# Performance work log

Measured on AMD Instinct MI355X. Metric: run time of the kernel, lower is better.

The kernel has to match this reference:

```python
import jax, jax.numpy as jnp
import numpy as np

N, IN_C, HID, OUT_C, DEPTH = 4096, 128, 256, 128, 3
KS = [2048, 1024, 512]  # ceil(0.5 * N_level)
E = 131072


def glorot(key, fan_in, fan_out):
    lim = np.sqrt(6.0 / (fan_in + fan_out))
    return jax.random.uniform(key, (fan_in, fan_out), jnp.float32, -lim, lim)


def build_adj(edge_index, n):
    # symmetric, self-loop-free adjacency with unit edge weights
    A = jnp.zeros((n, n), jnp.float32)
    A = A.at[edge_index[0], edge_index[1]].set(1.0)
    A = jnp.maximum(A, A.T)
    return A * (1.0 - jnp.eye(n, dtype=jnp.float32))


def gcn(x, A, W, b):
    # GCNConv(improved=True): A_hat = A + 2I, symmetric normalization
    n = A.shape[0]
    Ah = A + 2.0 * jnp.eye(n, dtype=A.dtype)
    deg = Ah.sum(axis=1)
    dinv = jnp.where(deg > 0, deg ** -0.5, 0.0)
    An = dinv[:, None] * Ah * dinv[None, :]
    return An @ (x @ W) + b


def augment(A):
    # remove self loops, add self loops (w=1), square (spspmm), remove self loops
    n = A.shape[0]
    I = jnp.eye(n, dtype=A.dtype)
    Al = A * (1.0 - I) + I
    A2 = Al @ Al
    return A2 * (1.0 - I)


def topk_pool(x, A, p, k):
    score = jnp.tanh((x @ p) / jnp.linalg.norm(p))
    vals, perm = jax.lax.top_k(score, k)
    return x[perm] * vals[:, None], A[perm][:, perm], perm


def setup_inputs() -> dict:
    key = jax.random.key(0)
    ks = jax.random.split(key, 16)
    x = jax.random.normal(ks[0], (N, IN_C), jnp.float32)
    edge_index = jax.random.randint(ks[1], (2, E), 0, N, jnp.int32)
    d = {"x": x, "edge_index": edge_index}
    d["Wd0"], d["bd0"] = glorot(ks[2], IN_C, HID), jnp.zeros((HID,), jnp.float32)
    d["Wd1"], d["bd1"] = glorot(ks[3], HID, HID), jnp.zeros((HID,), jnp.float32)
    d["Wd2"], d["bd2"] = glorot(ks[4], HID, HID), jnp.zeros((HID,), jnp.float32)
    d["Wd3"], d["bd3"] = glorot(ks[5], HID, HID), jnp.zeros((HID,), jnp.float32)
    d["p1"] = jax.random.normal(ks[6], (HID,), jnp.float32)
    d["p2"] = jax.random.normal(ks[7], (HID,), jnp.float32)
    d["p3"] = jax.random.normal(ks[8], (HID,), jnp.float32)
    d["Wu0"], d["bu0"] = glorot(ks[9], HID, HID), jnp.zeros((HID,), jnp.float32)
    d["Wu1"], d["bu1"] = glorot(ks[10], HID, HID), jnp.zeros((HID,), jnp.float32)
    d["Wu2"], d["bu2"] = glorot(ks[11], HID, OUT_C), jnp.zeros((OUT_C,), jnp.float32)
    return d


def reference(x, edge_index, Wd0, bd0, Wd1, bd1, Wd2, bd2, Wd3, bd3,
              p1, p2, p3, Wu0, bu0, Wu1, bu1, Wu2, bu2):
    n = x.shape[0]
    A = build_adj(edge_index, n)
    x = jax.nn.relu(gcn(x, A, Wd0, bd0))
    xs, As, perms = [x], [A], []
    down = [(Wd1, bd1), (Wd2, bd2), (Wd3, bd3)]
    pools = [p1, p2, p3]
    for i in range(DEPTH):
        A = augment(A)
        x, A, perm = topk_pool(x, A, pools[i], KS[i])
        x = jax.nn.relu(gcn(x, A, *down[i]))
        if i < DEPTH - 1:
            xs.append(x)
            As.append(A)
        perms.append(perm)
    up = [(Wu0, bu0), (Wu1, bu1), (Wu2, bu2)]
    for i in range(DEPTH):
        j = DEPTH - 1 - i
        res, perm = xs[j], perms[j]
        u = jnp.zeros_like(res).at[perm].set(x)
        x = res + u  # sum_res=True
        x = gcn(x, As[j], *up[i])
        if i < DEPTH - 1:
            x = jax.nn.relu(x)
    return x
```

## Files before the change

kernel.cpp:

```cpp
#include <hip/hip_runtime.h>


typedef __attribute__((ext_vector_type(8))) short bf16x8;
typedef __attribute__((ext_vector_type(4))) short s16x4;
typedef __attribute__((ext_vector_type(4))) float f32x4;

__device__ __forceinline__ short f2bf(float f) {
    unsigned u = __builtin_bit_cast(unsigned, f);
    u += 0x7FFFu + ((u >> 16) & 1u);
    return (short)(u >> 16);
}
__device__ __forceinline__ float bf2f(short s) {
    unsigned u = ((unsigned)(unsigned short)s) << 16;
    return __builtin_bit_cast(float, u);
}

#define GLL16(gsrc, ldst)                                                        \
    __builtin_amdgcn_global_load_lds(                                            \
        (__attribute__((address_space(1))) void*)(gsrc),                         \
        (__attribute__((address_space(3))) void*)(ldst), 16, 0, 0)

template<int MODE, int EPI>
__global__ __launch_bounds__(256, 2)
void gemm_bt(const short* __restrict__ Ah, const short* __restrict__ Al,
             const short* __restrict__ Bh, const short* __restrict__ Bl,
             float* __restrict__ Cf, int M, int N, int K, int kChunk)
{
    if (EPI == 1 && (int)blockIdx.y > (int)blockIdx.x) return;

    __shared__ short sAh[128 * 32];
    __shared__ short sBh[128 * 32];
    __shared__ short sAl[(MODE == 2) ? 128 * 32 : 8];
    __shared__ short sBl[(MODE >= 1) ? 128 * 32 : 8];

    const int t    = threadIdx.x;
    const int lane = t & 63;
    const int wave = t >> 6;
    const int tM   = blockIdx.y * 128;
    const int tN   = blockIdx.x * 128;
    const int k0   = blockIdx.z * kChunk;

    const int wm  = (wave >> 1) * 64;
    const int wn  = (wave & 1) * 64;
    const int l15 = lane & 15;
    const int g8  = (lane >> 4) * 8;

    f32x4 acc[4][4];
    const f32x4 zero = {0.f, 0.f, 0.f, 0.f};
#pragma unroll
    for (int i = 0; i < 4; i++)
#pragma unroll
        for (int j = 0; j < 4; j++) acc[i][j] = zero;

    const int i0 = t, i1 = t + 256;
    const short* a0 = Ah + (size_t)(tM + (i0 >> 2)) * K + (i0 & 3) * 8;
    const short* a1 = Ah + (size_t)(tM + (i1 >> 2)) * K + (i1 & 3) * 8;
    const short* b0 = Bh + (size_t)(tN + (i0 >> 2)) * K + (i0 & 3) * 8;
    const short* b1 = Bh + (size_t)(tN + (i1 >> 2)) * K + (i1 & 3) * 8;
    const short *bl0 = nullptr, *bl1 = nullptr, *al0 = nullptr, *al1 = nullptr;
    if (MODE >= 1) {
        bl0 = Bl + (size_t)(tN + (i0 >> 2)) * K + (i0 & 3) * 8;
        bl1 = Bl + (size_t)(tN + (i1 >> 2)) * K + (i1 & 3) * 8;
    }
    if (MODE == 2) {
        al0 = Al + (size_t)(tM + (i0 >> 2)) * K + (i0 & 3) * 8;
        al1 = Al + (size_t)(tM + (i1 >> 2)) * K + (i1 & 3) * 8;
    }

    for (int kb = k0; kb < k0 + kChunk; kb += 32) {
        GLL16(a0 + kb, &sAh[i0 * 8]);
        GLL16(a1 + kb, &sAh[i1 * 8]);
        GLL16(b0 + kb, &sBh[i0 * 8]);
        GLL16(b1 + kb, &sBh[i1 * 8]);
        if (MODE >= 1) { GLL16(bl0 + kb, &sBl[i0 * 8]); GLL16(bl1 + kb, &sBl[i1 * 8]); }
        if (MODE == 2) { GLL16(al0 + kb, &sAl[i0 * 8]); GLL16(al1 + kb, &sAl[i1 * 8]); }
        __syncthreads();

        bf16x8 aF[4], bF[4], aL[4], bL[4];
#pragma unroll
        for (int i = 0; i < 4; i++)
            aF[i] = *(const bf16x8*)&sAh[(wm + i * 16 + l15) * 32 + g8];
#pragma unroll
        for (int j = 0; j < 4; j++)
            bF[j] = *(const bf16x8*)&sBh[(wn + j * 16 + l15) * 32 + g8];
        if (MODE >= 1)
#pragma unroll
            for (int j = 0; j < 4; j++)
                bL[j] = *(const bf16x8*)&sBl[(wn + j * 16 + l15) * 32 + g8];
        if (MODE == 2)
#pragma unroll
            for (int i = 0; i < 4; i++)
                aL[i] = *(const bf16x8*)&sAl[(wm + i * 16 + l15) * 32 + g8];

#pragma unroll
        for (int i = 0; i < 4; i++)
#pragma unroll
            for (int j = 0; j < 4; j++) {
                acc[i][j] = __builtin_amdgcn_mfma_f32_16x16x32_bf16(aF[i], bF[j], acc[i][j], 0, 0, 0);
                if (MODE >= 1)
                    acc[i][j] = __builtin_amdgcn_mfma_f32_16x16x32_bf16(aF[i], bL[j], acc[i][j], 0, 0, 0);
                if (MODE == 2)
                    acc[i][j] = __builtin_amdgcn_mfma_f32_16x16x32_bf16(aL[i], bF[j], acc[i][j], 0, 0, 0);
            }
        __syncthreads();
    }

    const int r4 = (lane >> 4) * 4;
    if (EPI == 3) {
        float* CT = Cf + (size_t)blockIdx.z * M * N;
#pragma unroll
        for (int i = 0; i < 4; i++)
#pragma unroll
            for (int j = 0; j < 4; j++) {
                const int col   = tN + wn + j * 16 + l15;
                const int rbase = tM + wm + i * 16 + r4;
                *(f32x4*)&CT[(size_t)col * M + rbase] = acc[i][j];
            }
    } else {
        float* Cg = Cf + (size_t)blockIdx.z * M * N;
#pragma unroll
        for (int i = 0; i < 4; i++)
#pragma unroll
            for (int j = 0; j < 4; j++) {
                const int col = tN + wn + j * 16 + l15;
                float* cp = Cg + (size_t)(tM + wm + i * 16 + r4) * N + col;
#pragma unroll
                for (int r = 0; r < 4; r++) cp[(size_t)r * N] = acc[i][j][r];
            }
        if (EPI == 1 && tM != tN) {
#pragma unroll
            for (int i = 0; i < 4; i++)
#pragma unroll
                for (int j = 0; j < 4; j++) {
                    const int col   = tN + wn + j * 16 + l15;
                    const int rbase = tM + wm + i * 16 + r4;
                    *(f32x4*)&Cg[(size_t)col * N + rbase] = acc[i][j];
                }
        }
    }
}


__global__ void prep(const float* __restrict__ Wd0, const float* __restrict__ Wd1,
                     const float* __restrict__ Wd2, const float* __restrict__ Wd3,
                     const float* __restrict__ Wu0, const float* __restrict__ Wu1,
                     const float* __restrict__ Wu2, const float* __restrict__ x0,
                     short* __restrict__ Wth, short* __restrict__ Wtl,
                     short* __restrict__ Xh, short* __restrict__ Xl,
                     unsigned long long* __restrict__ M0)
{
    int t = blockIdx.x * 256 + threadIdx.x;
    float v; int dst;
    if (t < 32768)       { int e = t;          v = Wd0[e]; dst = 0      + (e & 255) * 128 + (e >> 8); }
    else if (t < 98304)  { int e = t - 32768;  v = Wd1[e]; dst = 32768  + (e & 255) * 256 + (e >> 8); }
    else if (t < 163840) { int e = t - 98304;  v = Wd2[e]; dst = 98304  + (e & 255) * 256 + (e >> 8); }
    else if (t < 229376) { int e = t - 163840; v = Wd3[e]; dst = 163840 + (e & 255) * 256 + (e >> 8); }
    else if (t < 294912) { int e = t - 229376; v = Wu0[e]; dst = 229376 + (e & 255) * 256 + (e >> 8); }
    else if (t < 360448) { int e = t - 294912; v = Wu1[e]; dst = 294912 + (e & 255) * 256 + (e >> 8); }
    else if (t < 393216) { int e = t - 360448; v = Wu2[e]; dst = 360448 + (e & 127) * 256 + (e >> 7); }
    else if (t < 917504) {
        int e = t - 393216;
        v = x0[e];
        short h = f2bf(v);
        Xh[e] = h; Xl[e] = f2bf(v - bf2f(h));
        return;
    } else {
        M0[t - 917504] = 0ull;
        return;
    }
    short h = f2bf(v);
    Wth[dst] = h; Wtl[dst] = f2bf(v - bf2f(h));
}

__global__ void build_bits(const int* __restrict__ ei, int E,
                           unsigned long long* __restrict__ M0)
{
    int e = blockIdx.x * 256 + threadIdx.x;
    if (e >= E) return;
    int i = ei[e], j = ei[E + e];
    if (i != j) {
        atomicOr(&M0[(size_t)i * 64 + (j >> 6)], 1ull << (j & 63));
        atomicOr(&M0[(size_t)j * 64 + (i >> 6)], 1ull << (i & 63));
    }
}

__global__ void row_compact_bits(const unsigned long long* __restrict__ M0,
                                 int* __restrict__ csr, float* __restrict__ rs)
{
    int row = blockIdx.x * 4 + (threadIdx.x >> 6);
    int lane = threadIdx.x & 63;
    unsigned long long w = M0[(size_t)row * 64 + lane];
    int c = __popcll(w);
    int incl = c;
    for (int off = 1; off < 64; off <<= 1) {
        int v = __shfl_up(incl, off);
        if (lane >= off) incl += v;
    }
    int base = incl - c;
    int* out = csr + (size_t)row * 128;
    while (w) {
        int b = __ffsll((unsigned long long)w) - 1;
        if (base < 128) out[base] = lane * 64 + b;
        base++;
        w &= w - 1;
    }
    if (lane == 63) rs[row] = (float)incl;
}

__global__ void mask_gather(const unsigned long long* __restrict__ M0,
                            const int* __restrict__ perm,
                            unsigned long long* __restrict__ mask,
                            float* __restrict__ rs, int kk)
{
    int t = blockIdx.x * 256 + threadIdx.x;
    if (t < kk) rs[t] = 0.f;
    int r = t >> 6, l = t & 63;
    int u = perm[r];
    unsigned long long w = M0[(size_t)u * 64 + l];
    if ((u >> 6) == l) w |= 1ull << (u & 63);
    mask[t] = w;
}

#define PSTR2 18
__global__ __launch_bounds__(256, 8)
void popc_aug_p(const unsigned long long* __restrict__ mask,
                short* __restrict__ Cp)
{
    const int bx = blockIdx.x, by = blockIdx.y, z = blockIdx.z;
    if (by > bx) return;
    __shared__ unsigned long long a[64 * PSTR2];
    __shared__ unsigned long long b[64 * PSTR2];
    const int t = threadIdx.x;
#pragma unroll
    for (int p = 0; p < 4; p++) {
        int idx = p * 256 + t;
        int rr = idx >> 4, w = idx & 15;
        a[rr * PSTR2 + w] = mask[((size_t)(by * 64 + rr)) * 64 + z * 16 + w];
        b[rr * PSTR2 + w] = mask[((size_t)(bx * 64 + rr)) * 64 + z * 16 + w];
    }
    __syncthreads();
    const int i0 = (t >> 4) * 4;
    const int j0 = t & 15;
    int acc[4][4];
#pragma unroll
    for (int qi = 0; qi < 4; qi++)
#pragma unroll
        for (int qj = 0; qj < 4; qj++) acc[qi][qj] = 0;
#pragma unroll
    for (int w = 0; w < 16; w += 2) {
        ulong2 av[4], bv[4];
#pragma unroll
        for (int q = 0; q < 4; q++) av[q] = *(const ulong2*)&a[(i0 + q) * PSTR2 + w];
#pragma unroll
        for (int q = 0; q < 4; q++) bv[q] = *(const ulong2*)&b[(j0 + 16 * q) * PSTR2 + w];
#pragma unroll
        for (int qi = 0; qi < 4; qi++)
#pragma unroll
            for (int qj = 0; qj < 4; qj++) {
                acc[qi][qj] += __builtin_popcountll(av[qi].x & bv[qj].x);
                acc[qi][qj] += __builtin_popcountll(av[qi].y & bv[qj].y);
            }
    }
    short* out = Cp + ((size_t)z * 1024 + (size_t)(by * 32 + bx)) * 4096;
#pragma unroll
    for (int qi = 0; qi < 4; qi++)
#pragma unroll
        for (int qj = 0; qj < 4; qj++)
            out[(i0 + qi) * 64 + j0 + 16 * qj] = (short)acc[qi][qj];
}

__global__ __launch_bounds__(256)
void aug_merge(const short* __restrict__ Cp, int kk,
               short* __restrict__ Ahs, float* __restrict__ rs)
{
    const int bx = blockIdx.x, by = blockIdx.y;
    if (by > bx) return;
    __shared__ float tile[64][65];
    __shared__ float rsum[64], csum[64];
    const int t = threadIdx.x;
    const int i  = t >> 2;
    const int c0 = (t & 3) * 16;
    const size_t tb = (size_t)(by * 32 + bx) * 4096;
    const size_t ss = (size_t)1024 * 4096;
    if (t < 64) { rsum[t] = 0.f; csum[t] = 0.f; }

    int v[16];
#pragma unroll
    for (int q = 0; q < 16; q++) v[q] = 0;
    for (int s = 0; s < 4; s++) {
        bf16x8 p0 = *(const bf16x8*)&Cp[tb + s * ss + i * 64 + c0];
        bf16x8 p1 = *(const bf16x8*)&Cp[tb + s * ss + i * 64 + c0 + 8];
#pragma unroll
        for (int q = 0; q < 8; q++) { v[q] += (int)p0[q]; v[8 + q] += (int)p1[q]; }
    }
    const int gi = by * 64 + i;
    float rp = 0.f;
    s16x4 pk[4];
#pragma unroll
    for (int q = 0; q < 16; q++) {
        const int gj = bx * 64 + c0 + q;
        float val = (gi == gj) ? 0.f : (float)v[q];
        tile[i][c0 + q] = val;
        rp += val;
        pk[q >> 2][q & 3] = f2bf(val);
    }
#pragma unroll
    for (int q = 0; q < 4; q++)
        *(s16x4*)&Ahs[(size_t)gi * kk + bx * 64 + c0 + q * 4] = pk[q];
    __syncthreads();
    atomicAdd(&rsum[i], rp);
    if (bx != by) {
        float cpv = 0.f;
#pragma unroll
        for (int q = 0; q < 16; q++) {
            float val = tile[c0 + q][i];
            cpv += val;
            pk[q >> 2][q & 3] = f2bf(val);
        }
#pragma unroll
        for (int q = 0; q < 4; q++)
            *(s16x4*)&Ahs[(size_t)(bx * 64 + i) * kk + by * 64 + c0 + q * 4] = pk[q];
        atomicAdd(&csum[i], cpv);
    }
    __syncthreads();
    if (t < 64) {
        atomicAdd(&rs[by * 64 + t], rsum[t]);
        if (bx != by) atomicAdd(&rs[bx * 64 + t], csum[t]);
    }
}

__global__ void z_reduce(const float* __restrict__ Cp, int S,
                         const float* __restrict__ rs,
                         short* __restrict__ Zh, short* __restrict__ Zl,
                         int n, int C)
{
    int t4 = (blockIdx.x * 256 + threadIdx.x) * 4;
    int r = t4 % n;
    size_t stride = (size_t)n * C;
    f32x4 v = {0.f, 0.f, 0.f, 0.f};
    for (int s = 0; s < S; s++) v += *(const f32x4*)&Cp[t4 + s * stride];
    f32x4 rsv = *(const f32x4*)&rs[r];
    s16x4 zh, zl;
#pragma unroll
    for (int q = 0; q < 4; q++) {
        float z = v[q] / sqrtf(rsv[q] + 2.f);
        short h = f2bf(z);
        zh[q] = h; zl[q] = f2bf(z - bf2f(h));
    }
    *(s16x4*)&Zh[t4] = zh;
    *(s16x4*)&Zl[t4] = zl;
}

__global__ void zf_reduce(const float* __restrict__ Cp, int S,
                          const float* __restrict__ rs,
                          float* __restrict__ Zf, int n, int C)
{
    int t4 = (blockIdx.x * 256 + threadIdx.x) * 4;
    int r = t4 / C;
    size_t stride = (size_t)n * C;
    f32x4 v = {0.f, 0.f, 0.f, 0.f};
    for (int s = 0; s < S; s++) v += *(const f32x4*)&Cp[t4 + s * stride];
    float d = 1.f / sqrtf(rs[r] + 2.f);
    v *= d;
    *(f32x4*)&Zf[t4] = v;
}

template<int CN, int RELU, int SC>
__global__ __launch_bounds__(256)
void spmm_gcn(const int* __restrict__ csr, const float* __restrict__ rs,
              const float* __restrict__ Zf, const float* __restrict__ b,
              float* __restrict__ out,
              const float* __restrict__ pvec, float* __restrict__ score)
{
    const int lane = threadIdx.x & 63;
    const int row  = blockIdx.x * 4 + (threadIdx.x >> 6);
    const int dg   = (int)rs[row];
    const int* nb  = csr + (size_t)row * 128;
    if (CN == 256) {
        const int c = lane * 4;
        float4 acc = {0.f, 0.f, 0.f, 0.f};
        int q = 0;
        for (; q + 4 <= dg; q += 4) {
            int j0 = nb[q], j1 = nb[q+1], j2 = nb[q+2], j3 = nb[q+3];
            float4 z0 = *(const float4*)&Zf[(size_t)j0 * CN + c];
            float4 z1 = *(const float4*)&Zf[(size_t)j1 * CN + c];
            float4 z2 = *(const float4*)&Zf[(size_t)j2 * CN + c];
            float4 z3 = *(const float4*)&Zf[(size_t)j3 * CN + c];
            acc.x += z0.x; acc.y += z0.y; acc.z += z0.z; acc.w += z0.w;
            acc.x += z1.x; acc.y += z1.y; acc.z += z1.z; acc.w += z1.w;
            acc.x += z2.x; acc.y += z2.y; acc.z += z2.z; acc.w += z2.w;
            acc.x += z3.x; acc.y += z3.y; acc.z += z3.z; acc.w += z3.w;
        }
        for (; q < dg; q++) {
            float4 z = *(const float4*)&Zf[(size_t)nb[q] * CN + c];
            acc.x += z.x; acc.y += z.y; acc.z += z.z; acc.w += z.w;
        }
        float d = 1.f / sqrtf(rs[row] + 2.f);
        float4 zi = *(const float4*)&Zf[(size_t)row * CN + c];
        float4 bb = *(const float4*)&b[c];
        float4 g;
        g.x = d * acc.x + 2.f * d * zi.x + bb.x;
        g.y = d * acc.y + 2.f * d * zi.y + bb.y;
        g.z = d * acc.z + 2.f * d * zi.z + bb.z;
        g.w = d * acc.w + 2.f * d * zi.w + bb.w;
        if (RELU) {
            g.x = fmaxf(g.x, 0.f); g.y = fmaxf(g.y, 0.f);
            g.z = fmaxf(g.z, 0.f); g.w = fmaxf(g.w, 0.f);
        }
        *(float4*)&out[(size_t)row * CN + c] = g;
        if (SC) {
            float4 pv = ((const float4*)pvec)[lane];
            double nn  = (double)pv.x * pv.x + (double)pv.y * pv.y +
                         (double)pv.z * pv.z + (double)pv.w * pv.w;
            double acd = (double)g.x * pv.x + (double)g.y * pv.y +
                         (double)g.z * pv.z + (double)g.w * pv.w;
            for (int off = 32; off; off >>= 1) {
                acd += __shfl_down(acd, off);
                nn  += __shfl_down(nn, off);
            }
            if (lane == 0) score[row] = tanhf((float)(acd / sqrt(nn)));
        }
    } else {
        const int c = lane * 2;
        float2 acc = {0.f, 0.f};
        int q = 0;
        for (; q + 4 <= dg; q += 4) {
            int j0 = nb[q], j1 = nb[q+1], j2 = nb[q+2], j3 = nb[q+3];
            float2 z0 = *(const float2*)&Zf[(size_t)j0 * CN + c];
            float2 z1 = *(const float2*)&Zf[(size_t)j1 * CN + c];
            float2 z2 = *(const float2*)&Zf[(size_t)j2 * CN + c];
            float2 z3 = *(const float2*)&Zf[(size_t)j3 * CN + c];
            acc.x += z0.x; acc.y += z0.y;
            acc.x += z1.x; acc.y += z1.y;
            acc.x += z2.x; acc.y += z2.y;
            acc.x += z3.x; acc.y += z3.y;
        }
        for (; q < dg; q++) {
            float2 z = *(const float2*)&Zf[(size_t)nb[q] * CN + c];
            acc.x += z.x; acc.y += z.y;
        }
        float d = 1.f / sqrtf(rs[row] + 2.f);
        float2 zi = *(const float2*)&Zf[(size_t)row * CN + c];
        float2 g;
        g.x = d * acc.x + 2.f * d * zi.x + b[c];
        g.y = d * acc.y + 2.f * d * zi.y + b[c + 1];
        if (RELU) { g.x = fmaxf(g.x, 0.f); g.y = fmaxf(g.y, 0.f); }
        *(float2*)&out[(size_t)row * CN + c] = g;
    }
}

template<int SC>
__global__ void gcn_final(const float* __restrict__ Cp, int S,
                          const short* __restrict__ Zh, const short* __restrict__ Zl,
                          const float* __restrict__ rs, const float* __restrict__ b,
                          float* __restrict__ out, short* __restrict__ oh,
                          short* __restrict__ ol, int k, int C, int relu,
                          const int* __restrict__ inv, const float* __restrict__ res,
                          const float* __restrict__ pvec, float* __restrict__ score)
{
    int t4 = (blockIdx.x * 256 + threadIdx.x) * 4;
    int j = t4 / C, c = t4 - j * C;
    int r = inv ? inv[j] : j;
    f32x4 v = res ? *(const f32x4*)&res[t4] : (f32x4){0.f, 0.f, 0.f, 0.f};
    if (r >= 0) {
        size_t base = (size_t)r * C + c;
        size_t stride = (size_t)k * C;
        f32x4 az = {0.f, 0.f, 0.f, 0.f};
        for (int s = 0; s < S; s++) az += *(const f32x4*)&Cp[base + s * stride];
        float d = 1.f / sqrtf(rs[r] + 2.f);
        f32x4 bb = *(const f32x4*)&b[c];
#pragma unroll
        for (int q = 0; q < 4; q++) {
            size_t zi = (size_t)(c + q) * k + r;
            float zz = bf2f(Zh[zi]) + bf2f(Zl[zi]);
            float g = d * az[q] + 2.f * d * zz + bb[q];
            if (relu && g < 0.f) g = 0.f;
            v[q] += g;
        }
    }
    *(f32x4*)&out[t4] = v;
    if (oh) {
        s16x4 hh, ll;
#pragma unroll
        for (int q = 0; q < 4; q++) {
            short h = f2bf(v[q]);
            hh[q] = h; ll[q] = f2bf(v[q] - bf2f(h));
        }
        *(s16x4*)&oh[t4] = hh;
        *(s16x4*)&ol[t4] = ll;
    }
    if (SC) {
        const int lane = threadIdx.x & 63;
        float4 pv = *(const float4*)&pvec[c];
        double nn  = (double)pv.x * pv.x + (double)pv.y * pv.y +
                     (double)pv.z * pv.z + (double)pv.w * pv.w;
        double acd = (double)v[0] * pv.x + (double)v[1] * pv.y +
                     (double)v[2] * pv.z + (double)v[3] * pv.w;
        for (int off = 32; off; off >>= 1) {
            acd += __shfl_down(acd, off);
            nn  += __shfl_down(nn, off);
        }
        if (lane == 0) score[j] = tanhf((float)(acd / sqrt(nn)));
    }
}

__device__ __forceinline__ unsigned long long packkey(float s, int i) {
    unsigned u = __builtin_bit_cast(unsigned, s);
    u = (u & 0x80000000u) ? ~u : (u | 0x80000000u);
    return ((unsigned long long)u << 32) | (unsigned)(0xFFFFFFFFu - (unsigned)i);
}

__global__ __launch_bounds__(512)
void rank_pool(const float* __restrict__ score, int n, int k,
               const float* __restrict__ xold,
               int* __restrict__ perm, int* __restrict__ inv,
               short* __restrict__ Xh, short* __restrict__ Xl)
{
    __shared__ unsigned long long sk[512];
    __shared__ int rk[64];
    __shared__ int selrow[64];
    __shared__ int selrank[64];
    __shared__ float selval[64];
    __shared__ int cnt;
    const int t  = threadIdx.x;
    const int il = t & 63;
    const int js = t >> 6;
    const int i  = blockIdx.x * 64 + il;
    if (t < 64) rk[t] = 0;
    if (t == 0) cnt = 0;
    const unsigned long long mykey = packkey(score[i], i);
    int r = 0;
    for (int jb = 0; jb < n; jb += 512) {
        __syncthreads();
        if (jb + t < n) sk[t] = packkey(score[jb + t], jb + t);
        __syncthreads();
        const unsigned long long* p = &sk[js * 64];
#pragma unroll 16
        for (int q = 0; q < 64; q++) r += (p[q] > mykey) ? 1 : 0;
    }
    atomicAdd(&rk[il], r);
    __syncthreads();
    if (t < 64) {
        int rank = rk[t];
        int ii = blockIdx.x * 64 + t;
        inv[ii] = (rank < k) ? rank : -1;
        if (rank < k) {
            perm[rank] = ii;
            int s = atomicAdd(&cnt, 1);
            selrow[s]  = ii;
            selrank[s] = rank;
            selval[s]  = score[ii];
        }
    }
    __syncthreads();
    const int wave = t >> 6, lane = t & 63;
    for (int s = wave; s < cnt; s += 8) {
        const int   row = selrow[s];
        const float vv  = selval[s];
        f32x4 x = *(const f32x4*)&xold[(size_t)row * 256 + lane * 4];
        s16x4 hh, ll;
#pragma unroll
        for (int q = 0; q < 4; q++) {
            float v = x[q] * vv;
            short h = f2bf(v);
            hh[q] = h; ll[q] = f2bf(v - bf2f(h));
        }
        size_t o = (size_t)selrank[s] * 256 + lane * 4;
        *(s16x4*)&Xh[o] = hh;
        *(s16x4*)&Xl[o] = ll;
    }
}

__global__ void gatherG_h(const short* __restrict__ A, int n,
                          const int* __restrict__ perm,
                          short* __restrict__ Gh, int kk,
                          float* __restrict__ rsz)
{
    int idx = blockIdx.x * 256 + threadIdx.x;
    if (idx < kk) rsz[idx] = 0.f;
    int t8 = idx * 8;
    if (t8 >= kk * n) return;
    int r = t8 / n, c0 = t8 - r * n;
    int pr = perm[r];
    bf16x8 a = *(const bf16x8*)&A[(size_t)pr * n + c0];
    if (pr >= c0 && pr < c0 + 8)
        a[pr - c0] = f2bf(bf2f(a[pr - c0]) + 1.f);
    *(bf16x8*)&Gh[t8] = a;
}

__global__ void gatherG_hl(const short* __restrict__ Ahi, const short* __restrict__ Alo,
                           int n, const int* __restrict__ perm,
                           short* __restrict__ Gh, short* __restrict__ Gl, int kk,
                           float* __restrict__ rsz)
{
    int idx = blockIdx.x * 256 + threadIdx.x;
    if (idx < kk) rsz[idx] = 0.f;
    int t8 = idx * 8;
    if (t8 >= kk * n) return;
    int r = t8 / n, c0 = t8 - r * n;
    int pr = perm[r];
    bf16x8 ah = *(const bf16x8*)&Ahi[(size_t)pr * n + c0];
    bf16x8 al = *(const bf16x8*)&Alo[(size_t)pr * n + c0];
    bf16x8 gh, gl;
#pragma unroll
    for (int q = 0; q < 8; q++) {
        float v = bf2f(ah[q]) + bf2f(al[q]) + ((c0 + q == pr) ? 1.f : 0.f);
        short h = f2bf(v);
        gh[q] = h; gl[q] = f2bf(v - bf2f(h));
    }
    *(bf16x8*)&Gh[t8] = gh;
    *(bf16x8*)&Gl[t8] = gl;
}

template<bool LO>
__global__ void aug_finish_f(const float* __restrict__ Cp, int S, int kk,
                             short* __restrict__ Ahs, short* __restrict__ Als,
                             float* __restrict__ rs)
{
    int t4 = (blockIdx.x * 256 + threadIdx.x) * 4;
    int r = t4 / kk, c0 = t4 - r * kk;
    size_t stride = (size_t)kk * kk;
    f32x4 v = {0.f, 0.f, 0.f, 0.f};
    for (int s = 0; s < S; s++) v += *(const f32x4*)&Cp[t4 + s * stride];
    if (r >= c0 && r < c0 + 4) v[r - c0] = 0.f;
    s16x4 hh, ll;
    float ws = 0.f;
#pragma unroll
    for (int q = 0; q < 4; q++) {
        short h = f2bf(v[q]);
        hh[q] = h;
        if (LO) ll[q] = f2bf(v[q] - bf2f(h));
        ws += v[q];
    }
    *(s16x4*)&Ahs[t4] = hh;
    if (LO) *(s16x4*)&Als[t4] = ll;
    for (int off = 32; off; off >>= 1) ws += __shfl_down(ws, off);
    if ((threadIdx.x & 63) == 0) atomicAdd(&rs[r], ws);
}


extern "C" void kernel_launch(void* const* d_in, const int* in_sizes, int n_in,
                              void* d_out, int out_size, void* d_ws, size_t ws_size,
                              hipStream_t stream)
{
    const float* x0  = (const float*)d_in[0];
    const int*   ei  = (const int*)d_in[1];
    const float* Wd0 = (const float*)d_in[2];  const float* bd0 = (const float*)d_in[3];
    const float* Wd1 = (const float*)d_in[4];  const float* bd1 = (const float*)d_in[5];
    const float* Wd2 = (const float*)d_in[6];  const float* bd2 = (const float*)d_in[7];
    const float* Wd3 = (const float*)d_in[8];  const float* bd3 = (const float*)d_in[9];
    const float* p1  = (const float*)d_in[10];
    const float* p2  = (const float*)d_in[11];
    const float* p3  = (const float*)d_in[12];
    const float* Wu0 = (const float*)d_in[13]; const float* bu0 = (const float*)d_in[14];
    const float* Wu1 = (const float*)d_in[15]; const float* bu1 = (const float*)d_in[16];
    const float* Wu2 = (const float*)d_in[17]; const float* bu2 = (const float*)d_in[18];

    const int E = in_sizes[1] / 2;

    char* ws = (char*)d_ws;
    size_t off = 0;
    auto alloc = [&](size_t bytes) -> void* {
        void* p = ws + off;
        off += (bytes + 255) & ~(size_t)255;
        return p;
    };
    unsigned long long* M0 = (unsigned long long*)alloc((size_t)4096 * 64 * 8);
    short* A1h  = (short*)alloc((size_t)2048 * 2048 * 2);
    short* A2h  = (short*)alloc((size_t)1024 * 1024 * 2);
    short* A2l  = (short*)alloc((size_t)1024 * 1024 * 2);
    short* A3h  = (short*)alloc((size_t)512 * 512 * 2);
    short* A3l  = (short*)alloc((size_t)512 * 512 * 2);
    short* Gh   = (short*)alloc((size_t)1024 * 2048 * 2);
    short* Gl   = (short*)alloc((size_t)512 * 1024 * 2);
    int*   csr  = (int*)alloc((size_t)4096 * 128 * 4);
    unsigned long long* maskb = (unsigned long long*)alloc((size_t)2048 * 64 * 8);
    float* Zf   = (float*)alloc((size_t)4096 * 256 * 4);
    float* Cp   = (float*)alloc((size_t)64 * 1024 * 1024);
    float* xs0  = (float*)alloc((size_t)4096 * 256 * 4);
    float* xs1  = (float*)alloc((size_t)2048 * 256 * 4);
    float* xs2  = (float*)alloc((size_t)1024 * 256 * 4);
    float* xu0  = (float*)alloc((size_t)4096 * 256 * 4);
    float* xu1  = (float*)alloc((size_t)2048 * 256 * 4);
    float* xu2  = (float*)alloc((size_t)1024 * 256 * 4);
    short* xu0h = (short*)alloc((size_t)4096 * 256 * 2);
    short* xu0l = (short*)alloc((size_t)4096 * 256 * 2);
    short* xu1h = (short*)alloc((size_t)2048 * 256 * 2);
    short* xu1l = (short*)alloc((size_t)2048 * 256 * 2);
    short* xu2h = (short*)alloc((size_t)1024 * 256 * 2);
    short* xu2l = (short*)alloc((size_t)1024 * 256 * 2);
    short* X0h  = (short*)alloc((size_t)4096 * 128 * 2);
    short* X0l  = (short*)alloc((size_t)4096 * 128 * 2);
    short* xah  = (short*)alloc((size_t)2048 * 256 * 2);
    short* xal  = (short*)alloc((size_t)2048 * 256 * 2);
    short* Wth  = (short*)alloc((size_t)393216 * 2);
    short* Wtl  = (short*)alloc((size_t)393216 * 2);
    short* Zh   = (short*)alloc((size_t)256 * 4096 * 2);
    short* Zl   = (short*)alloc((size_t)256 * 4096 * 2);
    float* rs0  = (float*)alloc(4096 * 4);
    float* rs1  = (float*)alloc(2048 * 4);
    float* rs2  = (float*)alloc(1024 * 4);
    float* rs3  = (float*)alloc(512 * 4);
    float* scoreb = (float*)alloc(4096 * 4);
    int*   perm1  = (int*)alloc(2048 * 4);
    int*   perm2  = (int*)alloc(1024 * 4);
    int*   perm3  = (int*)alloc(512 * 4);
    int*   inv1   = (int*)alloc(4096 * 4);
    int*   inv2   = (int*)alloc(2048 * 4);
    int*   inv3   = (int*)alloc(1024 * 4);

    auto gcn_dense = [&](const short* Xh, const short* Xl, int n, int Kc, int Cout,
                         const short* pAh, const short* pAl, const float* rsA,
                         int wtoff, const float* b,
                         float* out, short* oh, short* ol, int relu, int modeA,
                         int Saz, const int* inv, const float* res, int nout,
                         const float* pvec) {
        int Sxw = 4;
        gemm_bt<2, 3><<<dim3(Cout / 128, n / 128, Sxw), 256, 0, stream>>>(
            Xh, Xl, Wth + wtoff, Wtl + wtoff, Cp, n, Cout, Kc, Kc / Sxw);
        z_reduce<<<(n * Cout) / 1024, 256, 0, stream>>>(Cp, Sxw, rsA, Zh, Zl, n, Cout);
        dim3 g(Cout / 128, n / 128, Saz);
        if (modeA == 1)
            gemm_bt<1, 0><<<g, 256, 0, stream>>>(pAh, nullptr, Zh, Zl, Cp, n, Cout, n, n / Saz);
        else
            gemm_bt<2, 0><<<g, 256, 0, stream>>>(pAh, pAl, Zh, Zl, Cp, n, Cout, n, n / Saz);
        if (pvec)
            gcn_final<1><<<(nout * Cout) / 1024, 256, 0, stream>>>(
                Cp, Saz, Zh, Zl, rsA, b, out, oh, ol, n, Cout, relu, inv, res,
                pvec, scoreb);
        else
            gcn_final<0><<<(nout * Cout) / 1024, 256, 0, stream>>>(
                Cp, Saz, Zh, Zl, rsA, b, out, oh, ol, n, Cout, relu, inv, res,
                nullptr, nullptr);
    };

    auto pool = [&](const float* xlev, int n, int* perm, int* inv) {
        int k = n / 2;
        rank_pool<<<n / 64, 512, 0, stream>>>(scoreb, n, k, xlev, perm, inv, xah, xal);
    };

    prep<<<4608, 256, 0, stream>>>(Wd0, Wd1, Wd2, Wd3, Wu0, Wu1, Wu2, x0,
                                   Wth, Wtl, X0h, X0l, M0);
    build_bits<<<(E + 255) / 256, 256, 0, stream>>>(ei, E, M0);
    row_compact_bits<<<1024, 256, 0, stream>>>(M0, csr, rs0);

    gemm_bt<2, 0><<<dim3(2, 32, 4), 256, 0, stream>>>(
        X0h, X0l, Wth, Wtl, Cp, 4096, 256, 128, 32);
    zf_reduce<<<1024, 256, 0, stream>>>(Cp, 4, rs0, Zf, 4096, 256);
    spmm_gcn<256, 1, 1><<<1024, 256, 0, stream>>>(csr, rs0, Zf, bd0, xs0, p1, scoreb);

    pool(xs0, 4096, perm1, inv1);
    mask_gather<<<512, 256, 0, stream>>>(M0, perm1, maskb, rs1, 2048);
    popc_aug_p<<<dim3(32, 32, 4), 256, 0, stream>>>(maskb, (short*)Cp);
    aug_merge<<<dim3(32, 32), 256, 0, stream>>>((const short*)Cp, 2048, A1h, rs1);
    gcn_dense(xah, xal, 2048, 256, 256, A1h, nullptr, rs1, 32768, bd1,
              xs1, nullptr, nullptr, 1, 1, 8, nullptr, nullptr, 2048, p2);

    pool(xs1, 2048, perm2, inv2);
    gatherG_h<<<(1024 * 2048 / 8) / 256, 256, 0, stream>>>(A1h, 2048, perm2, Gh, 1024, rs2);
    gemm_bt<0, 1><<<dim3(8, 8, 8), 256, 0, stream>>>(Gh, nullptr, Gh, nullptr, Cp, 1024, 1024, 2048, 256);
    aug_finish_f<true><<<(1024 * 1024 / 4) / 256, 256, 0, stream>>>(Cp, 8, 1024, A2h, A2l, rs2);
    gcn_dense(xah, xal, 1024, 256, 256, A2h, A2l, rs2, 98304, bd2,
              xs2, nullptr, nullptr, 1, 2, 8, nullptr, nullptr, 1024, p3);

    pool(xs2, 1024, perm3, inv3);
    gatherG_hl<<<(512 * 1024 / 8) / 256, 256, 0, stream>>>(A2h, A2l, 1024, perm3, Gh, Gl, 512, rs3);
    gemm_bt<2, 1><<<dim3(4, 4, 8), 256, 0, stream>>>(Gh, Gl, Gh, Gl, Cp, 512, 512, 1024, 128);
    aug_finish_f<true><<<(512 * 512 / 4) / 256, 256, 0, stream>>>(Cp, 8, 512, A3h, A3l, rs3);

    gcn_dense(xah, xal, 512, 256, 256, A3h, A3l, rs3, 163840, bd3,
              xu2, xu2h, xu2l, 1, 2, 8, inv3, xs2, 1024, nullptr);

    gcn_dense(xu2h, xu2l, 1024, 256, 256, A2h, A2l, rs2, 229376, bu0,
              xu1, xu1h, xu1l, 1, 2, 8, inv2, xs1, 2048, nullptr);

    gcn_dense(xu1h, xu1l, 2048, 256, 256, A1h, nullptr, rs1, 294912, bu1,
              xu0, xu0h, xu0l, 1, 1, 8, inv1, xs0, 4096, nullptr);

    gemm_bt<2, 0><<<dim3(1, 32, 8), 256, 0, stream>>>(
        xu0h, xu0l, Wth + 360448, Wtl + 360448, Cp, 4096, 128, 256, 32);
    zf_reduce<<<512, 256, 0, stream>>>(Cp, 8, rs0, Zf, 4096, 128);
    spmm_gcn<128, 0, 0><<<1024, 256, 0, stream>>>(csr, rs0, Zf, bu2, (float*)d_out,
                                                  nullptr, nullptr);
}
```

Measured before the change: 440.5 us.

## Fuse degree scaling into X·W GEMM epilogue and fold mask gather into pooling

The small X·W GEMMs no longer use split-K with a separate reduction kernel. They now run with a single K chunk and apply the 1/sqrt(deg+2) scaling, plus the bf16 hi/lo split where needed, directly in new GEMM epilogues. The separate mask_gather kernel is merged into rank_pool, which now writes the gathered adjacency bit rows and zeroes the degree buffer. This removes several launches and the round trip of split-K partials through memory. In exchange the GEMMs launch far fewer blocks (as few as 32), which may leave most of the GPU's compute units idle.

```diff
diff --git a/kernel.cpp b/kernel.cpp
--- a/kernel.cpp
+++ b/kernel.cpp
@@ -24,7 +24,9 @@
 __global__ __launch_bounds__(256, 2)
 void gemm_bt(const short* __restrict__ Ah, const short* __restrict__ Al,
              const short* __restrict__ Bh, const short* __restrict__ Bl,
-             float* __restrict__ Cf, int M, int N, int K, int kChunk)
+             float* __restrict__ Cf, int M, int N, int K, int kChunk,
+             const float* __restrict__ rsA, short* __restrict__ Zho,
+             short* __restrict__ Zlo)
 {
     if (EPI == 1 && (int)blockIdx.y > (int)blockIdx.x) return;
 
@@ -116,6 +118,41 @@
                 const int rbase = tM + wm + i * 16 + r4;
                 *(f32x4*)&CT[(size_t)col * M + rbase] = acc[i][j];
             }
+    } else if (EPI == 4) {
+#pragma unroll
+        for (int i = 0; i < 4; i++) {
+            const int rbase = tM + wm + i * 16 + r4;
+            f32x4 rsv = *(const f32x4*)&rsA[rbase];
+#pragma unroll
+            for (int j = 0; j < 4; j++) {
+                const int col = tN + wn + j * 16 + l15;
+                s16x4 zh, zl;
+#pragma unroll
+                for (int q = 0; q < 4; q++) {
+                    float z = acc[i][j][q] / sqrtf(rsv[q] + 2.f);
+                    short h = f2bf(z);
+                    zh[q] = h; zl[q] = f2bf(z - bf2f(h));
+                }
+                *(s16x4*)&Zho[(size_t)col * M + rbase] = zh;
+                *(s16x4*)&Zlo[(size_t)col * M + rbase] = zl;
+            }
+        }
+    } else if (EPI == 5) {
+#pragma unroll
+        for (int i = 0; i < 4; i++) {
+            const int rbase = tM + wm + i * 16 + r4;
+            f32x4 rsv = *(const f32x4*)&rsA[rbase];
+            f32x4 dv;
+#pragma unroll
+            for (int q = 0; q < 4; q++) dv[q] = 1.f / sqrtf(rsv[q] + 2.f);
+#pragma unroll
+            for (int j = 0; j < 4; j++) {
+                const int col = tN + wn + j * 16 + l15;
+                float* cp = Cf + (size_t)rbase * N + col;
+#pragma unroll
+                for (int q = 0; q < 4; q++) cp[(size_t)q * N] = acc[i][j][q] * dv[q];
+            }
+        }
     } else {
         float* Cg = Cf + (size_t)blockIdx.z * M * N;
 #pragma unroll
@@ -207,20 +244,6 @@
     if (lane == 63) rs[row] = (float)incl;
 }
 
-__global__ void mask_gather(const unsigned long long* __restrict__ M0,
-                            const int* __restrict__ perm,
-                            unsigned long long* __restrict__ mask,
-                            float* __restrict__ rs, int kk)
-{
-    int t = blockIdx.x * 256 + threadIdx.x;
-    if (t < kk) rs[t] = 0.f;
-    int r = t >> 6, l = t & 63;
-    int u = perm[r];
-    unsigned long long w = M0[(size_t)u * 64 + l];
-    if ((u >> 6) == l) w |= 1ull << (u & 63);
-    mask[t] = w;
-}
-
 #define PSTR2 18
 __global__ __launch_bounds__(256, 8)
 void popc_aug_p(const unsigned long long* __restrict__ mask,
@@ -327,42 +350,6 @@
         atomicAdd(&rs[by * 64 + t], rsum[t]);
         if (bx != by) atomicAdd(&rs[bx * 64 + t], csum[t]);
     }
-}
-
-__global__ void z_reduce(const float* __restrict__ Cp, int S,
-                         const float* __restrict__ rs,
-                         short* __restrict__ Zh, short* __restrict__ Zl,
-                         int n, int C)
-{
-    int t4 = (blockIdx.x * 256 + threadIdx.x) * 4;
-    int r = t4 % n;
-    size_t stride = (size_t)n * C;
-    f32x4 v = {0.f, 0.f, 0.f, 0.f};
-    for (int s = 0; s < S; s++) v += *(const f32x4*)&Cp[t4 + s * stride];
-    f32x4 rsv = *(const f32x4*)&rs[r];
-    s16x4 zh, zl;
-#pragma unroll
-    for (int q = 0; q < 4; q++) {
-        float z = v[q] / sqrtf(rsv[q] + 2.f);
-        short h = f2bf(z);
-        zh[q] = h; zl[q] = f2bf(z - bf2f(h));
-    }
-    *(s16x4*)&Zh[t4] = zh;
-    *(s16x4*)&Zl[t4] = zl;
-}
-
-__global__ void zf_reduce(const float* __restrict__ Cp, int S,
-                          const float* __restrict__ rs,
-                          float* __restrict__ Zf, int n, int C)
-{
-    int t4 = (blockIdx.x * 256 + threadIdx.x) * 4;
-    int r = t4 / C;
-    size_t stride = (size_t)n * C;
-    f32x4 v = {0.f, 0.f, 0.f, 0.f};
-    for (int s = 0; s < S; s++) v += *(const f32x4*)&Cp[t4 + s * stride];
-    float d = 1.f / sqrtf(rs[r] + 2.f);
-    v *= d;
-    *(f32x4*)&Zf[t4] = v;
 }
 
 template<int CN, int RELU, int SC>
@@ -514,7 +501,10 @@
 void rank_pool(const float* __restrict__ score, int n, int k,
                const float* __restrict__ xold,
                int* __restrict__ perm, int* __restrict__ inv,
-               short* __restrict__ Xh, short* __restrict__ Xl)
+               short* __restrict__ Xh, short* __restrict__ Xl,
+               const unsigned long long* __restrict__ M0,
+               unsigned long long* __restrict__ maskb,
+               float* __restrict__ rsz, int kz)
 {
     __shared__ unsigned long long sk[512];
     __shared__ int rk[64];
@@ -528,6 +518,10 @@
     const int i  = blockIdx.x * 64 + il;
     if (t < 64) rk[t] = 0;
     if (t == 0) cnt = 0;
+    if (rsz) {
+        int gz = blockIdx.x * 512 + t;
+        if (gz < kz) rsz[gz] = 0.f;
+    }
     const unsigned long long mykey = packkey(score[i], i);
     int r = 0;
     for (int jb = 0; jb < n; jb += 512) {
@@ -568,6 +562,11 @@
         size_t o = (size_t)selrank[s] * 256 + lane * 4;
         *(s16x4*)&Xh[o] = hh;
         *(s16x4*)&Xl[o] = ll;
+        if (maskb) {
+            unsigned long long w = M0[(size_t)row * 64 + lane];
+            if ((row >> 6) == lane) w |= 1ull << (row & 63);
+            maskb[(size_t)selrank[s] * 64 + lane] = w;
+        }
     }
 }
 
@@ -715,15 +714,16 @@
                          float* out, short* oh, short* ol, int relu, int modeA,
                          int Saz, const int* inv, const float* res, int nout,
                          const float* pvec) {
-        int Sxw = 4;
-        gemm_bt<2, 3><<<dim3(Cout / 128, n / 128, Sxw), 256, 0, stream>>>(
-            Xh, Xl, Wth + wtoff, Wtl + wtoff, Cp, n, Cout, Kc, Kc / Sxw);
-        z_reduce<<<(n * Cout) / 1024, 256, 0, stream>>>(Cp, Sxw, rsA, Zh, Zl, n, Cout);
+        gemm_bt<2, 4><<<dim3(Cout / 128, n / 128, 1), 256, 0, stream>>>(
+            Xh, Xl, Wth + wtoff, Wtl + wtoff, nullptr, n, Cout, Kc, Kc,
+            rsA, Zh, Zl);
         dim3 g(Cout / 128, n / 128, Saz);
         if (modeA == 1)
-            gemm_bt<1, 0><<<g, 256, 0, stream>>>(pAh, nullptr, Zh, Zl, Cp, n, Cout, n, n / Saz);
+            gemm_bt<1, 0><<<g, 256, 0, stream>>>(pAh, nullptr, Zh, Zl, Cp, n, Cout, n, n / Saz,
+                                                 nullptr, nullptr, nullptr);
         else
-            gemm_bt<2, 0><<<g, 256, 0, stream>>>(pAh, pAl, Zh, Zl, Cp, n, Cout, n, n / Saz);
+            gemm_bt<2, 0><<<g, 256, 0, stream>>>(pAh, pAl, Zh, Zl, Cp, n, Cout, n, n / Saz,
+                                                 nullptr, nullptr, nullptr);
         if (pvec)
             gcn_final<1><<<(nout * Cout) / 1024, 256, 0, stream>>>(
                 Cp, Saz, Zh, Zl, rsA, b, out, oh, ol, n, Cout, relu, inv, res,
@@ -734,9 +734,11 @@
                 nullptr, nullptr);
     };
 
-    auto pool = [&](const float* xlev, int n, int* perm, int* inv) {
+    auto pool = [&](const float* xlev, int n, int* perm, int* inv,
+                    unsigned long long* mb, float* rsz, int kz) {
         int k = n / 2;
-        rank_pool<<<n / 64, 512, 0, stream>>>(scoreb, n, k, xlev, perm, inv, xah, xal);
+        rank_pool<<<n / 64, 512, 0, stream>>>(scoreb, n, k, xlev, perm, inv,
+                                              xah, xal, M0, mb, rsz, kz);
     };
 
     prep<<<4608, 256, 0, stream>>>(Wd0, Wd1, Wd2, Wd3, Wu0, Wu1, Wu2, x0,
@@ -744,28 +746,28 @@
     build_bits<<<(E + 255) / 256, 256, 0, stream>>>(ei, E, M0);
     row_compact_bits<<<1024, 256, 0, stream>>>(M0, csr, rs0);
 
-    gemm_bt<2, 0><<<dim3(2, 32, 4), 256, 0, stream>>>(
-        X0h, X0l, Wth, Wtl, Cp, 4096, 256, 128, 32);
-    zf_reduce<<<1024, 256, 0, stream>>>(Cp, 4, rs0, Zf, 4096, 256);
+    gemm_bt<2, 5><<<dim3(2, 32, 1), 256, 0, stream>>>(
+        X0h, X0l, Wth, Wtl, Zf, 4096, 256, 128, 128, rs0, nullptr, nullptr);
     spmm_gcn<256, 1, 1><<<1024, 256, 0, stream>>>(csr, rs0, Zf, bd0, xs0, p1, scoreb);
 
-    pool(xs0, 4096, perm1, inv1);
-    mask_gather<<<512, 256, 0, stream>>>(M0, perm1, maskb, rs1, 2048);
+    pool(xs0, 4096, perm1, inv1, maskb, rs1, 2048);
     popc_aug_p<<<dim3(32, 32, 4), 256, 0, stream>>>(maskb, (short*)Cp);
     aug_merge<<<dim3(32, 32), 256, 0, stream>>>((const short*)Cp, 2048, A1h, rs1);
     gcn_dense(xah, xal, 2048, 256, 256, A1h, nullptr, rs1, 32768, bd1,
               xs1, nullptr, nullptr, 1, 1, 8, nullptr, nullptr, 2048, p2);
 
-    pool(xs1, 2048, perm2, inv2);
+    pool(xs1, 2048, perm2, inv2, nullptr, nullptr, 0);
     gatherG_h<<<(1024 * 2048 / 8) / 256, 256, 0, stream>>>(A1h, 2048, perm2, Gh, 1024, rs2);
-    gemm_bt<0, 1><<<dim3(8, 8, 8), 256, 0, stream>>>(Gh, nullptr, Gh, nullptr, Cp, 1024, 1024, 2048, 256);
+    gemm_bt<0, 1><<<dim3(8, 8, 8), 256, 0, stream>>>(Gh, nullptr, Gh, nullptr, Cp, 1024, 1024, 2048, 256,
+                                                     nullptr, nullptr, nullptr);
     aug_finish_f<true><<<(1024 * 1024 / 4) / 256, 256, 0, stream>>>(Cp, 8, 1024, A2h, A2l, rs2);
     gcn_dense(xah, xal, 1024, 256, 256, A2h, A2l, rs2, 98304, bd2,
               xs2, nullptr, nullptr, 1, 2, 8, nullptr, nullptr, 1024, p3);
 
-    pool(xs2, 1024, perm3, inv3);
+    pool(xs2, 1024, perm3, inv3, nullptr, nullptr, 0);
     gatherG_hl<<<(512 * 1024 / 8) / 256, 256, 0, stream>>>(A2h, A2l, 1024, perm3, Gh, Gl, 512, rs3);
-    gemm_bt<2, 1><<<dim3(4, 4, 8), 256, 0, stream>>>(Gh, Gl, Gh, Gl, Cp, 512, 512, 1024, 128);
+    gemm_bt<2, 1><<<dim3(4, 4, 8), 256, 0, stream>>>(Gh, Gl, Gh, Gl, Cp, 512, 512, 1024, 128,
+                                                     nullptr, nullptr, nullptr);
     aug_finish_f<true><<<(512 * 512 / 4) / 256, 256, 0, stream>>>(Cp, 8, 512, A3h, A3l, rs3);
 
     gcn_dense(xah, xal, 512, 256, 256, A3h, A3l, rs3, 163840, bd3,
@@ -777,9 +779,9 @@
     gcn_dense(xu1h, xu1l, 2048, 256, 256, A1h, nullptr, rs1, 294912, bu1,
               xu0, xu0h, xu0l, 1, 1, 8, inv1, xs0, 4096, nullptr);
 
-    gemm_bt<2, 0><<<dim3(1, 32, 8), 256, 0, stream>>>(
-        xu0h, xu0l, Wth + 360448, Wtl + 360448, Cp, 4096, 128, 256, 32);
-    zf_reduce<<<512, 256, 0, stream>>>(Cp, 8, rs0, Zf, 4096, 128);
+    gemm_bt<2, 5><<<dim3(1, 32, 1), 256, 0, stream>>>(
+        xu0h, xu0l, Wth + 360448, Wtl + 360448, Zf, 4096, 128, 256, 256,
+        rs0, nullptr, nullptr);
     spmm_gcn<128, 0, 0><<<1024, 256, 0, stream>>>(csr, rs0, Zf, bu2, (float*)d_out,
                                                   nullptr, nullptr);
 }
```

Result: slower. 453.5 us (+3.0%).

## Fuse split-K bitmask popcount with augmentation merge into one kernel

Applied to the files above, without the earlier changes.

The popcount augmentation (A²) kernel and the merge kernel become a single kernel. Each block now loops over the four 16-word K slices, accumulates counts in registers, zeroes the diagonal, and writes both the bf16 tile and its transpose along with row sums. This removes the int16 partial-sum buffer's global write and read-back, plus one kernel launch. The cost is about a quarter as many blocks, each doing a serial K loop, and shared memory reused between the bitmask staging and the transpose tile.

```diff
diff --git a/kernel.cpp b/kernel.cpp
--- a/kernel.cpp
+++ b/kernel.cpp
@@ -223,22 +223,19 @@
 
 #define PSTR2 18
 __global__ __launch_bounds__(256, 8)
-void popc_aug_p(const unsigned long long* __restrict__ mask,
-                short* __restrict__ Cp)
-{
-    const int bx = blockIdx.x, by = blockIdx.y, z = blockIdx.z;
+void popc_aug_full(const unsigned long long* __restrict__ mask, int kk,
+                   short* __restrict__ Ahs, float* __restrict__ rs)
+{
+    const int bx = blockIdx.x, by = blockIdx.y;
     if (by > bx) return;
-    __shared__ unsigned long long a[64 * PSTR2];
-    __shared__ unsigned long long b[64 * PSTR2];
+    __shared__ unsigned long long smraw[2 * 64 * PSTR2];
+    unsigned long long* a = smraw;
+    unsigned long long* b = smraw + 64 * PSTR2;
+    float (*tile)[65] = (float (*)[65])smraw;
+    float* rsum = (float*)smraw + 64 * 65;
+    float* csum = rsum + 64;
+
     const int t = threadIdx.x;
-#pragma unroll
-    for (int p = 0; p < 4; p++) {
-        int idx = p * 256 + t;
-        int rr = idx >> 4, w = idx & 15;
-        a[rr * PSTR2 + w] = mask[((size_t)(by * 64 + rr)) * 64 + z * 16 + w];
-        b[rr * PSTR2 + w] = mask[((size_t)(bx * 64 + rr)) * 64 + z * 16 + w];
-    }
-    __syncthreads();
     const int i0 = (t >> 4) * 4;
     const int j0 = t & 15;
     int acc[4][4];
@@ -246,68 +243,60 @@
     for (int qi = 0; qi < 4; qi++)
 #pragma unroll
         for (int qj = 0; qj < 4; qj++) acc[qi][qj] = 0;
-#pragma unroll
-    for (int w = 0; w < 16; w += 2) {
-        ulong2 av[4], bv[4];
-#pragma unroll
-        for (int q = 0; q < 4; q++) av[q] = *(const ulong2*)&a[(i0 + q) * PSTR2 + w];
-#pragma unroll
-        for (int q = 0; q < 4; q++) bv[q] = *(const ulong2*)&b[(j0 + 16 * q) * PSTR2 + w];
-#pragma unroll
-        for (int qi = 0; qi < 4; qi++)
-#pragma unroll
-            for (int qj = 0; qj < 4; qj++) {
-                acc[qi][qj] += __builtin_popcountll(av[qi].x & bv[qj].x);
-                acc[qi][qj] += __builtin_popcountll(av[qi].y & bv[qj].y);
-            }
-    }
-    short* out = Cp + ((size_t)z * 1024 + (size_t)(by * 32 + bx)) * 4096;
+
+    for (int z = 0; z < 4; z++) {
+        __syncthreads();
+#pragma unroll
+        for (int p = 0; p < 4; p++) {
+            int idx = p * 256 + t;
+            int rr = idx >> 4, w = idx & 15;
+            a[rr * PSTR2 + w] = mask[((size_t)(by * 64 + rr)) * 64 + z * 16 + w];
+            b[rr * PSTR2 + w] = mask[((size_t)(bx * 64 + rr)) * 64 + z * 16 + w];
+        }
+        __syncthreads();
+#pragma unroll
+        for (int w = 0; w < 16; w += 2) {
+            ulong2 av[4], bv[4];
+#pragma unroll
+            for (int q = 0; q < 4; q++) av[q] = *(const ulong2*)&a[(i0 + q) * PSTR2 + w];
+#pragma unroll
+            for (int q = 0; q < 4; q++) bv[q] = *(const ulong2*)&b[(j0 + 16 * q) * PSTR2 + w];
+#pragma unroll
+            for (int qi = 0; qi < 4; qi++)
+#pragma unroll
+                for (int qj = 0; qj < 4; qj++) {
+                    acc[qi][qj] += __builtin_popcountll(av[qi].x & bv[qj].x);
+                    acc[qi][qj] += __builtin_popcountll(av[qi].y & bv[qj].y);
+                }
+        }
+    }
+
+    __syncthreads();
+    if (t < 64) { rsum[t] = 0.f; csum[t] = 0.f; }
 #pragma unroll
     for (int qi = 0; qi < 4; qi++)
 #pragma unroll
-        for (int qj = 0; qj < 4; qj++)
-            out[(i0 + qi) * 64 + j0 + 16 * qj] = (short)acc[qi][qj];
-}
-
-__global__ __launch_bounds__(256)
-void aug_merge(const short* __restrict__ Cp, int kk,
-               short* __restrict__ Ahs, float* __restrict__ rs)
-{
-    const int bx = blockIdx.x, by = blockIdx.y;
-    if (by > bx) return;
-    __shared__ float tile[64][65];
-    __shared__ float rsum[64], csum[64];
-    const int t = threadIdx.x;
+        for (int qj = 0; qj < 4; qj++) {
+            const int gi = by * 64 + i0 + qi;
+            const int gj = bx * 64 + j0 + 16 * qj;
+            tile[i0 + qi][j0 + 16 * qj] = (gi == gj) ? 0.f : (float)acc[qi][qj];
+        }
+    __syncthreads();
+
     const int i  = t >> 2;
     const int c0 = (t & 3) * 16;
-    const size_t tb = (size_t)(by * 32 + bx) * 4096;
-    const size_t ss = (size_t)1024 * 4096;
-    if (t < 64) { rsum[t] = 0.f; csum[t] = 0.f; }
-
-    int v[16];
-#pragma unroll
-    for (int q = 0; q < 16; q++) v[q] = 0;
-    for (int s = 0; s < 4; s++) {
-        bf16x8 p0 = *(const bf16x8*)&Cp[tb + s * ss + i * 64 + c0];
-        bf16x8 p1 = *(const bf16x8*)&Cp[tb + s * ss + i * 64 + c0 + 8];
-#pragma unroll
-        for (int q = 0; q < 8; q++) { v[q] += (int)p0[q]; v[8 + q] += (int)p1[q]; }
-    }
     const int gi = by * 64 + i;
     float rp = 0.f;
     s16x4 pk[4];
 #pragma unroll
     for (int q = 0; q < 16; q++) {
-        const int gj = bx * 64 + c0 + q;
-        float val = (gi == gj) ? 0.f : (float)v[q];
-        tile[i][c0 + q] = val;
+        float val = tile[i][c0 + q];
         rp += val;
         pk[q >> 2][q & 3] = f2bf(val);
     }
 #pragma unroll
     for (int q = 0; q < 4; q++)
         *(s16x4*)&Ahs[(size_t)gi * kk + bx * 64 + c0 + q * 4] = pk[q];
-    __syncthreads();
     atomicAdd(&rsum[i], rp);
     if (bx != by) {
         float cpv = 0.f;
@@ -751,8 +740,7 @@
 
     pool(xs0, 4096, perm1, inv1);
     mask_gather<<<512, 256, 0, stream>>>(M0, perm1, maskb, rs1, 2048);
-    popc_aug_p<<<dim3(32, 32, 4), 256, 0, stream>>>(maskb, (short*)Cp);
-    aug_merge<<<dim3(32, 32), 256, 0, stream>>>((const short*)Cp, 2048, A1h, rs1);
+    popc_aug_full<<<dim3(32, 32), 256, 0, stream>>>(maskb, 2048, A1h, rs1);
     gcn_dense(xah, xal, 2048, 256, 256, A1h, nullptr, rs1, 32768, bd1,
               xs1, nullptr, nullptr, 1, 1, 8, nullptr, nullptr, 2048, p2);
 
```

Result: slower. 465.9 us (+5.8%).
